# Performance work log

Hardware: AMD Instinct MI355X
Metric: run time of the kernel (lower is better)

Reference implementation:

```python
import jax, jax.numpy as jnp
import numpy as np

B, C, H, W = 2, 128, 64, 64
D_STATE = 16
EXPAND = 2
D_INNER = C * EXPAND          # 256
DT_RANK = -(-C // 16)         # 8
K = 4                         # scan directions
COMPRESS = 3
SQUEEZE = 30
EPS = 1e-5


def layernorm(x, g, b):
    mu = x.mean(-1, keepdims=True)
    xm = x - mu
    var = (xm * xm).mean(-1, keepdims=True)
    return xm * jax.lax.rsqrt(var + EPS) * g + b


def conv2d(x, w, bias, pad):
    y = jax.lax.conv_general_dilated(x, w, (1, 1), ((pad, pad), (pad, pad)),
                                     dimension_numbers=('NCHW', 'OIHW', 'NCHW'))
    return y + bias[None, :, None, None]


def selective_scan(xs, dts, A, Bs, Cs):
    # xs,dts: (B,K,D,L); A: (K,D,N); Bs,Cs: (B,K,N,L)
    dt_t = jnp.moveaxis(dts, -1, 0)
    x_t = jnp.moveaxis(xs, -1, 0)
    B_t = jnp.moveaxis(Bs, -1, 0)
    C_t = jnp.moveaxis(Cs, -1, 0)
    h0 = jnp.zeros(xs.shape[:3] + (A.shape[-1],), xs.dtype)

    def step(h, inp):
        dt_l, x_l, b_l, c_l = inp          # (B,K,D),(B,K,D),(B,K,N),(B,K,N)
        dA = jnp.exp(dt_l[..., None] * A)  # (B,K,D,N)
        h = dA * h + (dt_l * x_l)[..., None] * b_l[:, :, None, :]
        y = jnp.einsum('bkdn,bkn->bkd', h, c_l)
        return h, y

    _, ys = jax.lax.scan(step, h0, (dt_t, x_t, B_t, C_t))
    return jnp.moveaxis(ys, 0, -1)  # (B,K,D,L)


def ss2d(x, p):  # x: (B,H,W,C) -> (B,H,W,C)
    xz = x @ p['in_proj_w'].T
    xc, z = jnp.split(xz, 2, axis=-1)
    xc = xc.transpose(0, 3, 1, 2)  # (B,D,H,W)
    xc = jax.lax.conv_general_dilated(xc, p['conv_w'], (1, 1), ((1, 1), (1, 1)),
                                      feature_group_count=D_INNER,
                                      dimension_numbers=('NCHW', 'OIHW', 'NCHW'))
    xc = jax.nn.silu(xc + p['conv_b'][None, :, None, None])
    b, d, h, w = xc.shape
    L = h * w
    x_hw = xc.reshape(b, d, L)
    x_wh = xc.transpose(0, 1, 3, 2).reshape(b, d, L)
    xs = jnp.stack([x_hw, x_wh, x_hw[..., ::-1], x_wh[..., ::-1]], axis=1)  # (B,4,D,L)
    x_dbl = jnp.einsum('bkdl,kcd->bkcl', xs, p['x_proj_w'])
    dtr, Bs, Cs = jnp.split(x_dbl, [DT_RANK, DT_RANK + D_STATE], axis=2)
    dts = jnp.einsum('bkrl,kdr->bkdl', dtr, p['dt_w'])
    dts = jax.nn.softplus(dts + p['dt_b'][None, :, :, None])
    A = -jnp.exp(p['A_logs']).reshape(K, d, D_STATE)
    ys = selective_scan(xs, dts, A, Bs, Cs)
    ys = ys + xs * p['Ds'].reshape(K, d)[None, :, :, None]
    inv = ys[:, 2:4][..., ::-1]  # undo flipped scans
    wh = lambda t: t.reshape(b, d, w, h).transpose(0, 1, 3, 2).reshape(b, d, L)
    y = ys[:, 0] + inv[:, 0] + wh(ys[:, 1]) + wh(inv[:, 1])
    y = y.transpose(0, 2, 1).reshape(b, h, w, d)
    y = layernorm(y, p['out_norm_g'], p['out_norm_b'])
    y = y * jax.nn.silu(z)
    return y @ p['out_proj_w'].T


def cab(x, p):  # x: (B,C,H,W)
    t = jax.nn.gelu(conv2d(x, p['cab_w1'], p['cab_b1'], 1), approximate=False)
    t = conv2d(t, p['cab_w2'], p['cab_b2'], 1)
    s = t.mean((2, 3), keepdims=True)
    s = jax.nn.relu(conv2d(s, p['ca_w1'], p['ca_b1'], 0))
    s = jax.nn.sigmoid(conv2d(s, p['ca_w2'], p['ca_b2'], 0))
    return t * s


def vss_block(input, p):
    inp = input.transpose(0, 2, 3, 1)  # (B,H,W,C)
    x = inp * p['skip_scale'] + ss2d(layernorm(inp, p['ln1_g'], p['ln1_b']), p)
    c = cab(layernorm(x, p['ln2_g'], p['ln2_b']).transpose(0, 3, 1, 2), p)
    x = x * p['skip_scale2'] + c.transpose(0, 2, 3, 1)
    return x.transpose(0, 3, 1, 2)


def setup_inputs() -> dict:
    key = jax.random.key(0)
    ks = jax.random.split(key, 16)
    rn = lambda i, shp, s=0.02: jax.random.normal(ks[i], shp, jnp.float32) * s
    return {
        'input': jax.random.normal(ks[0], (B, C, H, W), jnp.float32),
        'ln1_g': jnp.ones((C,), jnp.float32), 'ln1_b': jnp.zeros((C,), jnp.float32),
        'skip_scale': jnp.ones((C,), jnp.float32), 'skip_scale2': jnp.ones((C,), jnp.float32),
        'ln2_g': jnp.ones((C,), jnp.float32), 'ln2_b': jnp.zeros((C,), jnp.float32),
        'in_proj_w': rn(1, (2 * D_INNER, C)),
        'conv_w': rn(2, (D_INNER, 1, 3, 3), 0.1),
        'conv_b': jnp.zeros((D_INNER,), jnp.float32),
        'x_proj_w': rn(3, (K, DT_RANK + 2 * D_STATE, D_INNER)),
        'dt_w': rn(4, (K, D_INNER, DT_RANK), 0.1),
        'dt_b': rn(5, (K, D_INNER), 0.1),
        'A_logs': jnp.log(jnp.tile(jnp.arange(1, D_STATE + 1, dtype=jnp.float32), (K * D_INNER, 1))),
        'Ds': jnp.ones((K * D_INNER,), jnp.float32),
        'out_norm_g': jnp.ones((D_INNER,), jnp.float32), 'out_norm_b': jnp.zeros((D_INNER,), jnp.float32),
        'out_proj_w': rn(6, (C, D_INNER)),
        'cab_w1': rn(7, (C // COMPRESS, C, 3, 3), 0.05),
        'cab_b1': jnp.zeros((C // COMPRESS,), jnp.float32),
        'cab_w2': rn(8, (C, C // COMPRESS, 3, 3), 0.05),
        'cab_b2': jnp.zeros((C,), jnp.float32),
        'ca_w1': rn(9, (C // SQUEEZE, C, 1, 1), 0.05),
        'ca_b1': jnp.zeros((C // SQUEEZE,), jnp.float32),
        'ca_w2': rn(10, (C, C // SQUEEZE, 1, 1), 0.05),
        'ca_b2': jnp.zeros((C,), jnp.float32),
    }


def reference(input, ln1_g, ln1_b, skip_scale, skip_scale2, ln2_g, ln2_b,
              in_proj_w, conv_w, conv_b, x_proj_w, dt_w, dt_b, A_logs, Ds,
              out_norm_g, out_norm_b, out_proj_w,
              cab_w1, cab_b1, cab_w2, cab_b2, ca_w1, ca_b1, ca_w2, ca_b2):
    p = dict(ln1_g=ln1_g, ln1_b=ln1_b, skip_scale=skip_scale, skip_scale2=skip_scale2,
             ln2_g=ln2_g, ln2_b=ln2_b, in_proj_w=in_proj_w, conv_w=conv_w, conv_b=conv_b,
             x_proj_w=x_proj_w, dt_w=dt_w, dt_b=dt_b, A_logs=A_logs, Ds=Ds,
             out_norm_g=out_norm_g, out_norm_b=out_norm_b, out_proj_w=out_proj_w,
             cab_w1=cab_w1, cab_b1=cab_b1, cab_w2=cab_w2, cab_b2=cab_b2,
             ca_w1=ca_w1, ca_b1=ca_b1, ca_w2=ca_w2, ca_b2=ca_b2)
    return vss_block(input, p)
```

## Files before the change

### kernel.cpp

```cpp
#include <hip/hip_runtime.h>
#include <math.h>

#define BB 2
#define CC 128
#define HH 64
#define WW 64
#define LL 4096
#define DI 256
#define NS 16
#define KK 4
#define OC1 42

#define NC 256
#define CL 16

#define K3_POS 16
#define BCW 48

__device__ __forceinline__ float sigmoidf_(float x) { return 1.f / (1.f + __expf(-x)); }
__device__ __forceinline__ float siluf_(float x)    { return x * sigmoidf_(x); }

__device__ __forceinline__ int scan_pos(int k, int i) {
  if (k == 0) return i;
  if (k == 1) return ((i & 63) << 6) | (i >> 6);
  if (k == 2) return (LL - 1) - i;
  int j = (LL - 1) - i;
  return ((j & 63) << 6) | (j >> 6);
}

__global__ __launch_bounds__(256) void k1_ln_inproj(
    const float* __restrict__ inp, const float* __restrict__ g, const float* __restrict__ b,
    const float* __restrict__ wproj, float* __restrict__ xcin, float* __restrict__ zbuf) {
  __shared__ float sx[64][132];
  __shared__ float sw[128][68];
  __shared__ float smu[64], srs[64];
  const int tid = threadIdx.x;
  const int rt = blockIdx.x & 3;
  const int pt = blockIdx.x >> 2;
  const int bb = pt >> 6;
  const int pbase = (pt & 63) << 6;

  for (int idx = tid; idx < 64 * CC; idx += 256) {
    int c = idx >> 6, pl = idx & 63;
    sx[pl][c] = inp[((size_t)bb * CC + c) * LL + pbase + pl];
  }
  __syncthreads();
  {
    int pl = tid >> 2, j = tid & 3;
    float s = 0.f, s2 = 0.f;
    for (int c = j; c < CC; c += 4) { float v = sx[pl][c]; s += v; s2 += v * v; }
    s += __shfl_xor(s, 1); s2 += __shfl_xor(s2, 1);
    s += __shfl_xor(s, 2); s2 += __shfl_xor(s2, 2);
    if (j == 0) {
      float mu = s * (1.f / CC);
      smu[pl] = mu;
      srs[pl] = rsqrtf(s2 * (1.f / CC) - mu * mu + 1e-5f);
    }
  }
  __syncthreads();
  for (int idx = tid; idx < 64 * CC; idx += 256) {
    int c = idx & 127, pl = idx >> 7;
    sx[pl][c] = (sx[pl][c] - smu[pl]) * srs[pl] * g[c] + b[c];
  }

  const int pg = tid & 7, rg = tid >> 3;
  float acc[8][4];
#pragma unroll
  for (int j = 0; j < 8; j++)
#pragma unroll
    for (int q = 0; q < 4; q++) acc[j][q] = 0.f;

  for (int kc = 0; kc < CC; kc += 64) {
    __syncthreads();
    for (int idx = tid; idx < 128 * 64; idx += 256) {
      int cl = idx & 63, rl = idx >> 6;
      sw[rl][cl] = wproj[(size_t)(rt * 128 + rl) * CC + kc + cl];
    }
    __syncthreads();
#pragma unroll 4
    for (int i = 0; i < 16; i++) {
      const int k0 = kc + 4 * i, kl0 = 4 * i;
      float4 xv[8], wv[4];
#pragma unroll
      for (int j = 0; j < 8; j++) xv[j] = *(const float4*)&sx[pg + 8 * j][k0];
#pragma unroll
      for (int q = 0; q < 4; q++) wv[q] = *(const float4*)&sw[rg + 32 * q][kl0];
#pragma unroll
      for (int j = 0; j < 8; j++)
#pragma unroll
        for (int q = 0; q < 4; q++) {
          acc[j][q] += xv[j].x * wv[q].x + xv[j].y * wv[q].y
                     + xv[j].z * wv[q].z + xv[j].w * wv[q].w;
        }
    }
  }

  float* buf = (rt < 2) ? xcin : zbuf;
  const int drow = (rt & 1) * 128;
#pragma unroll
  for (int j = 0; j < 8; j++) {
    const int p = pbase + pg + 8 * j;
    float* dst = buf + ((size_t)bb * LL + p) * DI + drow;
#pragma unroll
    for (int q = 0; q < 4; q++) dst[rg + 32 * q] = acc[j][q];
  }
}

__global__ __launch_bounds__(256) void k2_dwconv(
    const float* __restrict__ xcin, const float* __restrict__ cw, const float* __restrict__ cb,
    float* __restrict__ xconv) {
  const int w0 = (blockIdx.x & 7) * 8;
  const int hh = (blockIdx.x >> 3) & 63;
  const int bb = blockIdx.x >> 9;
  const int d = threadIdx.x;

  float wv[9];
#pragma unroll
  for (int kk = 0; kk < 9; kk++) wv[kk] = cw[d * 9 + kk];
  const float bias = cb[d];

  float xin[3][10];
#pragma unroll
  for (int kh = 0; kh < 3; kh++) {
    int r = hh + kh - 1;
    bool vr = (r >= 0 && r < HH);
#pragma unroll
    for (int c = 0; c < 10; c++) {
      int cc2 = w0 + c - 1;
      bool vc = (cc2 >= 0 && cc2 < WW);
      xin[kh][c] = (vr && vc) ? xcin[((size_t)bb * LL + r * WW + cc2) * DI + d] : 0.f;
    }
  }
#pragma unroll
  for (int j = 0; j < 8; j++) {
    float acc = bias;
#pragma unroll
    for (int kh = 0; kh < 3; kh++)
#pragma unroll
      for (int kw = 0; kw < 3; kw++)
        acc += wv[kh * 3 + kw] * xin[kh][j + kw];
    xconv[((size_t)bb * LL + hh * WW + w0 + j) * DI + d] = siluf_(acc);
  }
}

__global__ __launch_bounds__(256) void k3_proj(
    const float* __restrict__ xconv, const float* __restrict__ xpw,
    float* __restrict__ BCbuf) {
  __shared__ float sx[16][68];
  __shared__ float sw[160][68];
  const int tid = threadIdx.x;
  const int bb = blockIdx.x >> 8;
  const int pbase = (blockIdx.x & 255) << 4;

  const int pg = tid & 7, rb = tid >> 3;
  float acc[2][5];
#pragma unroll
  for (int j = 0; j < 2; j++)
#pragma unroll
    for (int q = 0; q < 5; q++) acc[j][q] = 0.f;

  for (int kc = 0; kc < DI; kc += 64) {
    __syncthreads();
    for (int idx = tid; idx < 16 * 64; idx += 256) {
      int cl = idx & 63, pl = idx >> 6;
      sx[pl][cl] = xconv[((size_t)bb * LL + pbase + pl) * DI + kc + cl];
    }
    for (int idx = tid; idx < 160 * 64; idx += 256) {
      int cl = idx & 63, rl = idx >> 6;
      sw[rl][cl] = xpw[(size_t)rl * DI + kc + cl];
    }
    __syncthreads();
#pragma unroll 4
    for (int i = 0; i < 16; i++) {
      float4 xv[2], wv[5];
#pragma unroll
      for (int j = 0; j < 2; j++) xv[j] = *(const float4*)&sx[2 * pg + j][4 * i];
#pragma unroll
      for (int q = 0; q < 5; q++) wv[q] = *(const float4*)&sw[rb + 32 * q][4 * i];
#pragma unroll
      for (int j = 0; j < 2; j++)
#pragma unroll
        for (int q = 0; q < 5; q++) {
          acc[j][q] += xv[j].x * wv[q].x + xv[j].y * wv[q].y
                     + xv[j].z * wv[q].z + xv[j].w * wv[q].w;
        }
    }
  }

#pragma unroll
  for (int j = 0; j < 2; j++) {
    const int p = pbase + 2 * pg + j;
#pragma unroll
    for (int q = 0; q < 5; q++) {
      const int r = rb + 32 * q;
      const int k = r / 40, c0 = r - k * 40;
      BCbuf[((size_t)(bb * KK + k) * LL + p) * BCW + c0] = acc[j][q];
    }
  }
}

__global__ __launch_bounds__(256) void k4a_chunk(
    const float* __restrict__ xconv, const float* __restrict__ BCbuf,
    const float* __restrict__ A_logs, const float* __restrict__ dtw,
    const float* __restrict__ dtb,
    float* __restrict__ csS, float* __restrict__ csB) {
  __shared__ float sBC[CL][26];
  const int d = threadIdx.x;
  const int chunk = blockIdx.x & (NC - 1);
  const int t = blockIdx.x / NC;
  const int k = t & 3;
  const int bb = t >> 2;
  const int bk = bb * KK + k;
  const int base = chunk * CL;

  for (int idx = d; idx < CL * 24; idx += 256) {
    int ii = idx / 24, j = idx - ii * 24;
    int pos = scan_pos(k, base + ii);
    sBC[ii][j] = BCbuf[((size_t)bk * LL + pos) * BCW + j];
  }
  float a[NS];
  bool fast = true;
#pragma unroll
  for (int n = 0; n < NS; n++) {
    a[n] = -__expf(A_logs[((size_t)k * DI + d) * NS + n]);
    fast = fast && (fabsf(a[n] + (float)(n + 1)) < 1e-3f * (n + 1));
  }
  const float* wdt = dtw + ((size_t)k * DI + d) * 8;
  const float4 wd0 = *(const float4*)wdt;
  const float4 wd1 = *(const float4*)(wdt + 4);
  const float bdt = dtb[k * DI + d];
  __syncthreads();

  const float* x_p = xconv + (size_t)bb * LL * DI + d;

  float Bc[NS];
#pragma unroll
  for (int n = 0; n < NS; n++) Bc[n] = 0.f;
  float sumdt = 0.f;

  if (fast) {
#pragma unroll
    for (int half = 0; half < CL / 8; half++) {
      float xvr[8];
#pragma unroll
      for (int j = 0; j < 8; j++)
        xvr[j] = x_p[(size_t)scan_pos(k, base + half * 8 + j) * DI];
#pragma unroll
      for (int j = 0; j < 8; j++) {
        const int ii = half * 8 + j;
        const float* dr = sBC[ii];
        float u = bdt + wd0.x * dr[0] + wd0.y * dr[1] + wd0.z * dr[2] + wd0.w * dr[3]
                      + wd1.x * dr[4] + wd1.y * dr[5] + wd1.z * dr[6] + wd1.w * dr[7];
        float t2 = __expf(u);
        float E = __builtin_amdgcn_rcpf(1.f + t2);
        float dt = u > 20.f ? u : -0.69314718056f * __log2f(E);
        sumdt += dt;
        float dtx = dt * xvr[j];
        float E2 = E * E;
        float dA1 = E, dA2 = E2;
#pragma unroll
        for (int n = 0; n < NS; n += 2) {
          Bc[n] = dA1 * Bc[n] + dtx * sBC[ii][8 + n];
          Bc[n + 1] = dA2 * Bc[n + 1] + dtx * sBC[ii][9 + n];
          dA1 *= E2; dA2 *= E2;
        }
      }
    }
  } else {
#pragma unroll 2
    for (int ii = 0; ii < CL; ii++) {
      int pos = scan_pos(k, base + ii);
      float xv = x_p[(size_t)pos * DI];
      const float* dr = sBC[ii];
      float u = bdt + wd0.x * dr[0] + wd0.y * dr[1] + wd0.z * dr[2] + wd0.w * dr[3]
                    + wd1.x * dr[4] + wd1.y * dr[5] + wd1.z * dr[6] + wd1.w * dr[7];
      float t2 = __expf(u);
      float dt = u > 20.f ? u : log1pf(t2);
      sumdt += dt;
      float dtx = dt * xv;
#pragma unroll
      for (int n = 0; n < NS; n++) {
        float dA = __expf(dt * a[n]);
        Bc[n] = dA * Bc[n] + dtx * sBC[ii][8 + n];
      }
    }
  }
  csS[((size_t)bk * NC + chunk) * DI + d] = sumdt;
  size_t e = ((size_t)(bk * NC + chunk) * NS) * DI + d;
#pragma unroll
  for (int n = 0; n < NS; n++)
    csB[e + (size_t)n * DI] = Bc[n];
}

__global__ __launch_bounds__(256) void k4b_scanchunks(
    const float* __restrict__ csS, const float* __restrict__ csB,
    const float* __restrict__ A_logs, float* __restrict__ hin) {
  const int d = threadIdx.x;
  const int n = blockIdx.x & (NS - 1);
  const int bk = blockIdx.x >> 4;
  const int k = bk & 3;
  const float an = -__expf(A_logs[((size_t)k * DI + d) * NS + n]);
  const size_t strideB = (size_t)NS * DI;
  size_t e = ((size_t)bk * NC * NS + n) * DI + d;
  float H = 0.f;
  for (int c0 = 0; c0 < NC; c0 += 16) {
    float Ea[16], Bv[16];
#pragma unroll
    for (int j = 0; j < 16; j++) {
      Ea[j] = an * csS[((size_t)bk * NC + c0 + j) * DI + d];
      Bv[j] = csB[e + (size_t)j * strideB];
    }
#pragma unroll
    for (int j = 0; j < 16; j++) Ea[j] = __expf(Ea[j]);
#pragma unroll
    for (int j = 0; j < 16; j++) {
      hin[e + (size_t)j * strideB] = H;
      H = Ea[j] * H + Bv[j];
    }
    e += (size_t)16 * strideB;
  }
}

__global__ __launch_bounds__(256) void k4c_scan(
    const float* __restrict__ xconv, const float* __restrict__ BCbuf,
    const float* __restrict__ A_logs, const float* __restrict__ dtw,
    const float* __restrict__ dtb, const float* __restrict__ Ds,
    const float* __restrict__ hin, float* __restrict__ ys) {
  __shared__ float sBC[CL][BCW];
  const int d = threadIdx.x;
  const int chunk = blockIdx.x & (NC - 1);
  const int t = blockIdx.x / NC;
  const int k = t & 3;
  const int bb = t >> 2;
  const int bk = bb * KK + k;
  const int base = chunk * CL;

  for (int idx = d; idx < CL * 40; idx += 256) {
    int ii = idx / 40, j = idx - ii * 40;
    int pos = scan_pos(k, base + ii);
    sBC[ii][j] = BCbuf[((size_t)bk * LL + pos) * BCW + j];
  }
  float a[NS], h[NS];
  bool fast = true;
  const size_t eh = ((size_t)(bk * NC + chunk) * NS) * DI + d;
#pragma unroll
  for (int n = 0; n < NS; n++) {
    a[n] = -__expf(A_logs[((size_t)k * DI + d) * NS + n]);
    fast = fast && (fabsf(a[n] + (float)(n + 1)) < 1e-3f * (n + 1));
    h[n] = hin[eh + (size_t)n * DI];
  }
  const float* wdt = dtw + ((size_t)k * DI + d) * 8;
  const float4 wd0 = *(const float4*)wdt;
  const float4 wd1 = *(const float4*)(wdt + 4);
  const float bdt = dtb[k * DI + d];
  const float Dd = Ds[k * DI + d];
  __syncthreads();

  const float* x_p = xconv + (size_t)bb * LL * DI + d;
  float* ys_p = ys + (size_t)bk * LL * DI + d;

  if (fast) {
#pragma unroll
    for (int half = 0; half < CL / 8; half++) {
      float xvr[8];
#pragma unroll
      for (int j = 0; j < 8; j++)
        xvr[j] = x_p[(size_t)scan_pos(k, base + half * 8 + j) * DI];
#pragma unroll
      for (int j = 0; j < 8; j++) {
        const int ii = half * 8 + j;
        const float* dr = sBC[ii];
        float u = bdt + wd0.x * dr[0] + wd0.y * dr[1] + wd0.z * dr[2] + wd0.w * dr[3]
                      + wd1.x * dr[4] + wd1.y * dr[5] + wd1.z * dr[6] + wd1.w * dr[7];
        float t2 = __expf(u);
        float E = __builtin_amdgcn_rcpf(1.f + t2);
        float dt = u > 20.f ? u : -0.69314718056f * __log2f(E);
        float dtx = dt * xvr[j];
        float y = xvr[j] * Dd;
        float E2 = E * E;
        float dA1 = E, dA2 = E2;
#pragma unroll
        for (int n = 0; n < NS; n += 2) {
          h[n] = dA1 * h[n] + dtx * sBC[ii][8 + n];
          y += h[n] * sBC[ii][24 + n];
          h[n + 1] = dA2 * h[n + 1] + dtx * sBC[ii][9 + n];
          y += h[n + 1] * sBC[ii][25 + n];
          dA1 *= E2; dA2 *= E2;
        }
        ys_p[(size_t)scan_pos(k, base + ii) * DI] = y;
      }
    }
  } else {
#pragma unroll 2
    for (int ii = 0; ii < CL; ii++) {
      int pos = scan_pos(k, base + ii);
      float xv = x_p[(size_t)pos * DI];
      const float* dr = sBC[ii];
      float u = bdt + wd0.x * dr[0] + wd0.y * dr[1] + wd0.z * dr[2] + wd0.w * dr[3]
                    + wd1.x * dr[4] + wd1.y * dr[5] + wd1.z * dr[6] + wd1.w * dr[7];
      float t2 = __expf(u);
      float dt = u > 20.f ? u : log1pf(t2);
      float dtx = dt * xv;
      float y = xv * Dd;
#pragma unroll
      for (int n = 0; n < NS; n++) {
        float dA = __expf(dt * a[n]);
        h[n] = dA * h[n] + dtx * sBC[ii][8 + n];
        y += h[n] * sBC[ii][24 + n];
      }
      ys_p[(size_t)pos * DI] = y;
    }
  }
}

__global__ __launch_bounds__(256) void k5_fused(
    const float* __restrict__ ys, const float* __restrict__ zbuf,
    const float* __restrict__ ong, const float* __restrict__ onb,
    const float* __restrict__ opw,
    const float* __restrict__ inp, const float* __restrict__ sk,
    const float* __restrict__ g2, const float* __restrict__ b2,
    float* __restrict__ xres, float* __restrict__ ln2) {
  __shared__ float sy[16][260];
  __shared__ float sw[128][68];
  __shared__ float sr[16][132];
  __shared__ float smu[16], srs[16];
  const int tid = threadIdx.x;
  const int bb = blockIdx.x >> 8;
  const int pbase = (blockIdx.x & 255) << 4;

  for (int idx = tid; idx < 16 * DI; idx += 256) {
    int d = idx & 255, pl = idx >> 8;
    size_t o0 = (((size_t)bb * KK + 0) * LL + pbase + pl) * DI + d;
    const size_t st = (size_t)LL * DI;
    sy[pl][d] = ys[o0] + ys[o0 + st] + ys[o0 + 2 * st] + ys[o0 + 3 * st];
  }
  __syncthreads();
  {
    int pl = tid >> 4, j = tid & 15;
    float s = 0.f, s2 = 0.f;
    for (int d = j; d < DI; d += 16) { float v = sy[pl][d]; s += v; s2 += v * v; }
#pragma unroll
    for (int m = 1; m < 16; m <<= 1) { s += __shfl_xor(s, m); s2 += __shfl_xor(s2, m); }
    if (j == 0) {
      float mu = s * (1.f / DI);
      smu[pl] = mu;
      srs[pl] = rsqrtf(s2 * (1.f / DI) - mu * mu + 1e-5f);
    }
  }
  __syncthreads();
  for (int idx = tid; idx < 16 * DI; idx += 256) {
    int d = idx & 255, pl = idx >> 8;
    float zv = zbuf[((size_t)bb * LL + pbase + pl) * DI + d];
    sy[pl][d] = ((sy[pl][d] - smu[pl]) * srs[pl] * ong[d] + onb[d]) * siluf_(zv);
  }

  const int pg = tid & 7, rb = tid >> 3;
  float acc[2][4];
#pragma unroll
  for (int j = 0; j < 2; j++)
#pragma unroll
    for (int q = 0; q < 4; q++) acc[j][q] = 0.f;

  for (int kc = 0; kc < DI; kc += 64) {
    __syncthreads();
    for (int idx = tid; idx < 128 * 64; idx += 256) {
      int cl = idx & 63, rl = idx >> 6;
      sw[rl][cl] = opw[(size_t)rl * DI + kc + cl];
    }
    __syncthreads();
#pragma unroll 4
    for (int i = 0; i < 16; i++) {
      float4 xv[2], wv[4];
#pragma unroll
      for (int j = 0; j < 2; j++) xv[j] = *(const float4*)&sy[2 * pg + j][kc + 4 * i];
#pragma unroll
      for (int q = 0; q < 4; q++) wv[q] = *(const float4*)&sw[rb + 32 * q][4 * i];
#pragma unroll
      for (int j = 0; j < 2; j++)
#pragma unroll
        for (int q = 0; q < 4; q++) {
          acc[j][q] += xv[j].x * wv[q].x + xv[j].y * wv[q].y
                     + xv[j].z * wv[q].z + xv[j].w * wv[q].w;
        }
    }
  }

#pragma unroll
  for (int j = 0; j < 2; j++) {
    const int p = pbase + 2 * pg + j;
#pragma unroll
    for (int q = 0; q < 4; q++) {
      const int c = rb + 32 * q;
      float r = inp[((size_t)bb * CC + c) * LL + p] * sk[c] + acc[j][q];
      xres[((size_t)bb * LL + p) * CC + c] = r;
      sr[2 * pg + j][c] = r;
    }
  }
  __syncthreads();
  {
    int pl = tid >> 4, jj = tid & 15;
    float s = 0.f, s2 = 0.f;
    for (int c = jj; c < CC; c += 16) { float v = sr[pl][c]; s += v; s2 += v * v; }
#pragma unroll
    for (int m = 1; m < 16; m <<= 1) { s += __shfl_xor(s, m); s2 += __shfl_xor(s2, m); }
    if (jj == 0) {
      float mu = s * (1.f / CC);
      smu[pl] = mu;
      srs[pl] = rsqrtf(s2 * (1.f / CC) - mu * mu + 1e-5f);
    }
  }
  __syncthreads();
  for (int idx = tid; idx < 16 * CC; idx += 256) {
    int pl = idx & 15, c = idx >> 4;
    ln2[((size_t)bb * CC + c) * LL + pbase + pl] =
        (sr[pl][c] - smu[pl]) * srs[pl] * g2[c] + b2[c];
  }
}

__global__ __launch_bounds__(256) void k6a_conv1(
    const float* __restrict__ ln2, const float* __restrict__ w1,
    float* __restrict__ pc1) {
  __shared__ float sIn[16][6][68];
  __shared__ float sw[16 * 9 * OC1];
  const int tid = threadIdx.x;
  const int icq = blockIdx.x & 7;
  const int h4  = (blockIdx.x >> 3) & 15;
  const int bb  = blockIdx.x >> 7;
  const int icb = icq * 16;

  for (int idx = tid; idx < 16 * 6 * 66; idx += 256) {
    int i = idx / 396, rem = idx % 396;
    int rr = rem / 66, j = rem % 66;
    int r = h4 * 4 + rr - 1, c2 = j - 1;
    float v = 0.f;
    if (r >= 0 && r < HH && c2 >= 0 && c2 < WW)
      v = ln2[((size_t)bb * CC + icb + i) * LL + r * WW + c2];
    sIn[i][rr][j] = v;
  }
  for (int idx = tid; idx < OC1 * 16 * 9; idx += 256) {
    int oc = idx / 144, rem = idx % 144;
    int i = rem / 9, kk = rem % 9;
    sw[(i * 9 + kk) * OC1 + oc] = w1[((size_t)oc * CC + icb + i) * 9 + kk];
  }
  __syncthreads();

  const int wq = tid & 7, hq = (tid >> 3) & 3, ocg = tid >> 5;
  float acc[6][8];
#pragma unroll
  for (int q = 0; q < 6; q++)
#pragma unroll
    for (int ww = 0; ww < 8; ww++) acc[q][ww] = 0.f;

  for (int i = 0; i < 16; i++) {
    float xin[3][10];
#pragma unroll
    for (int kh = 0; kh < 3; kh++)
#pragma unroll
      for (int j = 0; j < 10; j++) xin[kh][j] = sIn[i][hq + kh][wq * 8 + j];
#pragma unroll
    for (int q = 0; q < 6; q++) {
      int oc = ocg + 8 * q;
      if (oc >= OC1) break;
      float wv[9];
#pragma unroll
      for (int kk = 0; kk < 9; kk++) wv[kk] = sw[(i * 9 + kk) * OC1 + oc];
#pragma unroll
      for (int kh = 0; kh < 3; kh++)
#pragma unroll
        for (int kw = 0; kw < 3; kw++)
#pragma unroll
          for (int ww = 0; ww < 8; ww++)
            acc[q][ww] += wv[kh * 3 + kw] * xin[kh][ww + kw];
    }
  }

  const int hrow = h4 * 4 + hq;
#pragma unroll
  for (int q = 0; q < 6; q++) {
    int oc = ocg + 8 * q;
    if (oc >= OC1) break;
    float* dst = pc1 + (((size_t)icq * BB + bb) * OC1 + oc) * LL + hrow * WW + wq * 8;
    *(float4*)dst       = make_float4(acc[q][0], acc[q][1], acc[q][2], acc[q][3]);
    *(float4*)(dst + 4) = make_float4(acc[q][4], acc[q][5], acc[q][6], acc[q][7]);
  }
}

__global__ __launch_bounds__(256) void k6b_reduce(
    const float* __restrict__ pc1, const float* __restrict__ b1,
    float* __restrict__ t1) {
  const int oc = blockIdx.x % OC1;
  const int bb = blockIdx.x / OC1;
  const float bias = b1[oc];
  const size_t st = (size_t)BB * OC1 * LL;
  const float* src = pc1 + ((size_t)bb * OC1 + oc) * LL;
  float* dst = t1 + ((size_t)bb * OC1 + oc) * LL;
  for (int i = threadIdx.x; i < LL / 4; i += 256) {
    float4 s = ((const float4*)src)[i];
#pragma unroll
    for (int icq = 1; icq < 8; icq++) {
      float4 v = *(const float4*)(src + (size_t)icq * st + i * 4);
      s.x += v.x; s.y += v.y; s.z += v.z; s.w += v.w;
    }
    float r[4] = {s.x + bias, s.y + bias, s.z + bias, s.w + bias};
#pragma unroll
    for (int q = 0; q < 4; q++)
      r[q] = 0.5f * r[q] * (1.f + erff(r[q] * 0.70710678118654752f));
    ((float4*)dst)[i] = make_float4(r[0], r[1], r[2], r[3]);
  }
}

__global__ __launch_bounds__(256) void k7_conv2(
    const float* __restrict__ t1, const float* __restrict__ w2,
    float* __restrict__ pc2) {
  __shared__ float sIn[21][4][68];
  __shared__ float swT[32 * 196];
  const int tid = threadIdx.x;
  const int icq = blockIdx.x & 1;
  const int h2  = (blockIdx.x >> 1) & 31;
  const int ocq = (blockIdx.x >> 6) & 3;
  const int bb  = blockIdx.x >> 8;
  const int icb = icq * 21;

  for (int idx = tid; idx < 21 * 4 * 66; idx += 256) {
    int i = idx / 264, rem = idx % 264;
    int rr = rem / 66, j = rem % 66;
    int r = h2 * 2 + rr - 1, c2 = j - 1;
    float v = 0.f;
    if (r >= 0 && r < HH && c2 >= 0 && c2 < WW)
      v = t1[((size_t)bb * OC1 + icb + i) * LL + r * WW + c2];
    sIn[i][rr][j] = v;
  }
  for (int idx = tid; idx < 32 * 189; idx += 256) {
    int ol = idx / 189, ikk = idx % 189;
    swT[ol * 196 + ikk] = w2[(size_t)(ocq * 32 + ol) * (OC1 * 9) + icb * 9 + ikk];
  }
  __syncthreads();

  const int wq = tid & 7, hq = (tid >> 3) & 1, ocg = tid >> 4;
  float acc[2][8];
#pragma unroll
  for (int q = 0; q < 2; q++)
#pragma unroll
    for (int ww = 0; ww < 8; ww++) acc[q][ww] = 0.f;

  for (int i = 0; i < 21; i++) {
    float xin[3][10];
#pragma unroll
    for (int kh = 0; kh < 3; kh++)
#pragma unroll
      for (int j = 0; j < 10; j++) xin[kh][j] = sIn[i][hq + kh][wq * 8 + j];
#pragma unroll
    for (int q = 0; q < 2; q++) {
      int ol = ocg + 16 * q;
      float wv[9];
#pragma unroll
      for (int kk = 0; kk < 9; kk++) wv[kk] = swT[ol * 196 + i * 9 + kk];
#pragma unroll
      for (int kh = 0; kh < 3; kh++)
#pragma unroll
        for (int kw = 0; kw < 3; kw++)
#pragma unroll
          for (int ww = 0; ww < 8; ww++)
            acc[q][ww] += wv[kh * 3 + kw] * xin[kh][ww + kw];
    }
  }

  const int hrow = h2 * 2 + hq;
#pragma unroll
  for (int q = 0; q < 2; q++) {
    int oc = ocq * 32 + ocg + 16 * q;
    float* dst = pc2 + (((size_t)icq * BB + bb) * CC + oc) * LL + hrow * WW + wq * 8;
    *(float4*)dst       = make_float4(acc[q][0], acc[q][1], acc[q][2], acc[q][3]);
    *(float4*)(dst + 4) = make_float4(acc[q][4], acc[q][5], acc[q][6], acc[q][7]);
  }
}

__global__ __launch_bounds__(256) void k8_mean(
    const float* __restrict__ pc2, const float* __restrict__ b2,
    float* __restrict__ t2, float* __restrict__ smean) {
  __shared__ float red[4];
  const int bc = blockIdx.x;
  const int bb = bc >> 7, c = bc & 127;
  const float bias = b2[c];
  const size_t st = (size_t)BB * CC * LL;
  const float* src = pc2 + ((size_t)bb * CC + c) * LL;
  float* dst = t2 + (size_t)bc * LL;
  float s = 0.f;
  for (int i = threadIdx.x; i < LL / 4; i += 256) {
    float4 v0 = ((const float4*)src)[i];
    float4 v1 = *(const float4*)(src + st + i * 4);
    float4 r = make_float4(v0.x + v1.x + bias, v0.y + v1.y + bias,
                           v0.z + v1.z + bias, v0.w + v1.w + bias);
    ((float4*)dst)[i] = r;
    s += r.x + r.y + r.z + r.w;
  }
#pragma unroll
  for (int m = 1; m < 64; m <<= 1) s += __shfl_xor(s, m);
  if ((threadIdx.x & 63) == 0) red[threadIdx.x >> 6] = s;
  __syncthreads();
  if (threadIdx.x == 0) smean[bc] = (red[0] + red[1] + red[2] + red[3]) * (1.f / LL);
}

__global__ __launch_bounds__(256) void k10_final(
    const float* __restrict__ xres, const float* __restrict__ t2,
    const float* __restrict__ smean,
    const float* __restrict__ cw1, const float* __restrict__ cb1,
    const float* __restrict__ cw2, const float* __restrict__ cb2,
    const float* __restrict__ sk2, float* __restrict__ out) {
  __shared__ float mid[4];
  const int tid = threadIdx.x;
  const int bc = blockIdx.x;
  const int bb = bc >> 7, c = bc & 127;

  {
    const int wv = tid >> 6, ln = tid & 63;
    float s = cw1[wv * CC + ln] * smean[bb * CC + ln]
            + cw1[wv * CC + 64 + ln] * smean[bb * CC + 64 + ln];
#pragma unroll
    for (int m = 1; m < 64; m <<= 1) s += __shfl_xor(s, m);
    if (ln == 0) mid[wv] = fmaxf(s + cb1[wv], 0.f);
  }
  __syncthreads();
  float a = cb2[c];
#pragma unroll
  for (int m = 0; m < 4; m++) a += cw2[c * 4 + m] * mid[m];
  const float sv = sigmoidf_(a);

  const float ss = sk2[c];
  const float* t2r = t2 + (size_t)bc * LL;
  float* outr = out + (size_t)bc * LL;
  for (int i = tid; i < LL; i += 256)
    outr[i] = xres[((size_t)bb * LL + i) * CC + c] * ss + t2r[i] * sv;
}


extern "C" void kernel_launch(void* const* d_in, const int* in_sizes, int n_in,
                              void* d_out, int out_size, void* d_ws, size_t ws_size,
                              hipStream_t stream) {
  const float* input      = (const float*)d_in[0];
  const float* ln1_g      = (const float*)d_in[1];
  const float* ln1_b      = (const float*)d_in[2];
  const float* skip_scale = (const float*)d_in[3];
  const float* skip_scale2= (const float*)d_in[4];
  const float* ln2_g      = (const float*)d_in[5];
  const float* ln2_b      = (const float*)d_in[6];
  const float* in_proj_w  = (const float*)d_in[7];
  const float* conv_w     = (const float*)d_in[8];
  const float* conv_b     = (const float*)d_in[9];
  const float* x_proj_w   = (const float*)d_in[10];
  const float* dt_w       = (const float*)d_in[11];
  const float* dt_b       = (const float*)d_in[12];
  const float* A_logs     = (const float*)d_in[13];
  const float* Ds         = (const float*)d_in[14];
  const float* out_norm_g = (const float*)d_in[15];
  const float* out_norm_b = (const float*)d_in[16];
  const float* out_proj_w = (const float*)d_in[17];
  const float* cab_w1     = (const float*)d_in[18];
  const float* cab_b1     = (const float*)d_in[19];
  const float* cab_w2     = (const float*)d_in[20];
  const float* cab_b2     = (const float*)d_in[21];
  const float* ca_w1      = (const float*)d_in[22];
  const float* ca_b1      = (const float*)d_in[23];
  const float* ca_w2      = (const float*)d_in[24];
  const float* ca_b2      = (const float*)d_in[25];

  float* ws = (float*)d_ws;
  float* xcin  = ws;
  float* zbuf  = xcin + (size_t)BB * LL * DI;
  float* xconv = zbuf + (size_t)BB * LL * DI;
  float* BCbuf = xconv + (size_t)BB * LL * DI;
  float* ysb   = BCbuf + (size_t)BB * KK * LL * BCW;
  float* xres  = ysb + (size_t)BB * KK * LL * DI;
  float* ln2b  = xres + (size_t)BB * LL * CC;
  float* t1b   = ln2b + (size_t)BB * CC * LL;
  float* t2b   = t1b + (size_t)BB * OC1 * LL;
  float* smean = t2b + (size_t)BB * CC * LL;
  float* hinbuf= smean + BB * CC;
  float* csS   = hinbuf + (size_t)BB * KK * NC * NS * DI;
  float* csB   = ysb;
  float* pc1   = ysb;
  float* pc2   = ysb + (size_t)3 * 1024 * 1024;

  k1_ln_inproj<<<512, 256, 0, stream>>>(input, ln1_g, ln1_b, in_proj_w, xcin, zbuf);
  k2_dwconv<<<BB * HH * (WW / 8), 256, 0, stream>>>(xcin, conv_w, conv_b, xconv);
  k3_proj<<<BB * (LL / K3_POS), 256, 0, stream>>>(xconv, x_proj_w, BCbuf);
  k4a_chunk<<<BB * KK * NC, 256, 0, stream>>>(xconv, BCbuf, A_logs, dt_w, dt_b, csS, csB);
  k4b_scanchunks<<<BB * KK * NS, 256, 0, stream>>>(csS, csB, A_logs, hinbuf);
  k4c_scan<<<BB * KK * NC, 256, 0, stream>>>(xconv, BCbuf, A_logs, dt_w, dt_b, Ds, hinbuf, ysb);
  k5_fused<<<BB * (LL / 16), 256, 0, stream>>>(ysb, zbuf, out_norm_g, out_norm_b, out_proj_w,
                                               input, skip_scale, ln2_g, ln2_b, xres, ln2b);
  k6a_conv1<<<BB * 16 * 8, 256, 0, stream>>>(ln2b, cab_w1, pc1);
  k6b_reduce<<<BB * OC1, 256, 0, stream>>>(pc1, cab_b1, t1b);
  k7_conv2<<<BB * 4 * 32 * 2, 256, 0, stream>>>(t1b, cab_w2, pc2);
  k8_mean<<<BB * CC, 256, 0, stream>>>(pc2, cab_b2, t2b, smean);
  k10_final<<<BB * CC, 256, 0, stream>>>(xres, t2b, smean, ca_w1, ca_b1, ca_w2, ca_b2,
                                         skip_scale2, (float*)d_out);
}
```

Baseline: 246.4 us.

## Store residual channel-major and drop split-K partials in second CAB conv

The residual is now written channel-major from the LayerNorm loop of the fused output-projection kernel, so the final kernel reads it contiguously instead of with a stride of 128. The second CAB convolution no longer splits input channels into two partial buffers. Each block covers all 42 input channels for 16 output channels, adds the bias and writes t2 directly, so the mean kernel only reduces. This removes one partial-sum round trip and the strided gather, but each conv2 thread now holds fewer output channels, which lowers weight and input reuse per load.

Measured after the change: 256.5 us. 4.1% more time.

```diff
diff --git a/kernel.cpp b/kernel.cpp
--- a/kernel.cpp
+++ b/kernel.cpp
@@ -419,7 +419,7 @@
     const float* __restrict__ opw,
     const float* __restrict__ inp, const float* __restrict__ sk,
     const float* __restrict__ g2, const float* __restrict__ b2,
-    float* __restrict__ xres, float* __restrict__ ln2) {
+    float* __restrict__ xresT, float* __restrict__ ln2) {
   __shared__ float sy[16][260];
   __shared__ float sw[128][68];
   __shared__ float sr[16][132];
@@ -492,7 +492,6 @@
     for (int q = 0; q < 4; q++) {
       const int c = rb + 32 * q;
       float r = inp[((size_t)bb * CC + c) * LL + p] * sk[c] + acc[j][q];
-      xres[((size_t)bb * LL + p) * CC + c] = r;
       sr[2 * pg + j][c] = r;
     }
   }
@@ -512,8 +511,10 @@
   __syncthreads();
   for (int idx = tid; idx < 16 * CC; idx += 256) {
     int pl = idx & 15, c = idx >> 4;
-    ln2[((size_t)bb * CC + c) * LL + pbase + pl] =
-        (sr[pl][c] - smu[pl]) * srs[pl] * g2[c] + b2[c];
+    float r = sr[pl][c];
+    size_t o = ((size_t)bb * CC + c) * LL + pbase + pl;
+    xresT[o] = r;
+    ln2[o] = (r - smu[pl]) * srs[pl] * g2[c] + b2[c];
   }
 }
 
@@ -611,88 +612,71 @@
 
 __global__ __launch_bounds__(256) void k7_conv2(
     const float* __restrict__ t1, const float* __restrict__ w2,
-    float* __restrict__ pc2) {
-  __shared__ float sIn[21][4][68];
-  __shared__ float swT[32 * 196];
+    const float* __restrict__ b2, float* __restrict__ t2) {
+  __shared__ float sIn[OC1][4][68];
+  __shared__ float swT[16 * 388];
   const int tid = threadIdx.x;
-  const int icq = blockIdx.x & 1;
-  const int h2  = (blockIdx.x >> 1) & 31;
-  const int ocq = (blockIdx.x >> 6) & 3;
+  const int h2  = blockIdx.x & 31;
+  const int ocq = (blockIdx.x >> 5) & 7;
   const int bb  = blockIdx.x >> 8;
-  const int icb = icq * 21;
-
-  for (int idx = tid; idx < 21 * 4 * 66; idx += 256) {
+
+  for (int idx = tid; idx < OC1 * 4 * 66; idx += 256) {
     int i = idx / 264, rem = idx % 264;
     int rr = rem / 66, j = rem % 66;
     int r = h2 * 2 + rr - 1, c2 = j - 1;
     float v = 0.f;
     if (r >= 0 && r < HH && c2 >= 0 && c2 < WW)
-      v = t1[((size_t)bb * OC1 + icb + i) * LL + r * WW + c2];
+      v = t1[((size_t)bb * OC1 + i) * LL + r * WW + c2];
     sIn[i][rr][j] = v;
   }
-  for (int idx = tid; idx < 32 * 189; idx += 256) {
-    int ol = idx / 189, ikk = idx % 189;
-    swT[ol * 196 + ikk] = w2[(size_t)(ocq * 32 + ol) * (OC1 * 9) + icb * 9 + ikk];
+  for (int idx = tid; idx < 16 * 378; idx += 256) {
+    int ol = idx / 378, ikk = idx % 378;
+    swT[ol * 388 + ikk] = w2[(size_t)(ocq * 16 + ol) * 378 + ikk];
   }
   __syncthreads();
 
   const int wq = tid & 7, hq = (tid >> 3) & 1, ocg = tid >> 4;
-  float acc[2][8];
-#pragma unroll
-  for (int q = 0; q < 2; q++)
-#pragma unroll
-    for (int ww = 0; ww < 8; ww++) acc[q][ww] = 0.f;
-
-  for (int i = 0; i < 21; i++) {
+  float acc[8];
+#pragma unroll
+  for (int ww = 0; ww < 8; ww++) acc[ww] = 0.f;
+
+  for (int i = 0; i < OC1; i++) {
     float xin[3][10];
 #pragma unroll
     for (int kh = 0; kh < 3; kh++)
 #pragma unroll
       for (int j = 0; j < 10; j++) xin[kh][j] = sIn[i][hq + kh][wq * 8 + j];
-#pragma unroll
-    for (int q = 0; q < 2; q++) {
-      int ol = ocg + 16 * q;
-      float wv[9];
-#pragma unroll
-      for (int kk = 0; kk < 9; kk++) wv[kk] = swT[ol * 196 + i * 9 + kk];
-#pragma unroll
-      for (int kh = 0; kh < 3; kh++)
-#pragma unroll
-        for (int kw = 0; kw < 3; kw++)
-#pragma unroll
-          for (int ww = 0; ww < 8; ww++)
-            acc[q][ww] += wv[kh * 3 + kw] * xin[kh][ww + kw];
-    }
+    float wv[9];
+#pragma unroll
+    for (int kk = 0; kk < 9; kk++) wv[kk] = swT[ocg * 388 + i * 9 + kk];
+#pragma unroll
+    for (int kh = 0; kh < 3; kh++)
+#pragma unroll
+      for (int kw = 0; kw < 3; kw++)
+#pragma unroll
+        for (int ww = 0; ww < 8; ww++)
+          acc[ww] += wv[kh * 3 + kw] * xin[kh][ww + kw];
   }
 
   const int hrow = h2 * 2 + hq;
-#pragma unroll
-  for (int q = 0; q < 2; q++) {
-    int oc = ocq * 32 + ocg + 16 * q;
-    float* dst = pc2 + (((size_t)icq * BB + bb) * CC + oc) * LL + hrow * WW + wq * 8;
-    *(float4*)dst       = make_float4(acc[q][0], acc[q][1], acc[q][2], acc[q][3]);
-    *(float4*)(dst + 4) = make_float4(acc[q][4], acc[q][5], acc[q][6], acc[q][7]);
-  }
+  const int oc = ocq * 16 + ocg;
+  const float bias = b2[oc];
+  float* dst = t2 + ((size_t)bb * CC + oc) * LL + hrow * WW + wq * 8;
+  *(float4*)dst       = make_float4(acc[0] + bias, acc[1] + bias,
+                                    acc[2] + bias, acc[3] + bias);
+  *(float4*)(dst + 4) = make_float4(acc[4] + bias, acc[5] + bias,
+                                    acc[6] + bias, acc[7] + bias);
 }
 
 __global__ __launch_bounds__(256) void k8_mean(
-    const float* __restrict__ pc2, const float* __restrict__ b2,
-    float* __restrict__ t2, float* __restrict__ smean) {
+    const float* __restrict__ t2, float* __restrict__ smean) {
   __shared__ float red[4];
   const int bc = blockIdx.x;
-  const int bb = bc >> 7, c = bc & 127;
-  const float bias = b2[c];
-  const size_t st = (size_t)BB * CC * LL;
-  const float* src = pc2 + ((size_t)bb * CC + c) * LL;
-  float* dst = t2 + (size_t)bc * LL;
+  const float* src = t2 + (size_t)bc * LL;
   float s = 0.f;
   for (int i = threadIdx.x; i < LL / 4; i += 256) {
-    float4 v0 = ((const float4*)src)[i];
-    float4 v1 = *(const float4*)(src + st + i * 4);
-    float4 r = make_float4(v0.x + v1.x + bias, v0.y + v1.y + bias,
-                           v0.z + v1.z + bias, v0.w + v1.w + bias);
-    ((float4*)dst)[i] = r;
-    s += r.x + r.y + r.z + r.w;
+    float4 v = ((const float4*)src)[i];
+    s += v.x + v.y + v.z + v.w;
   }
 #pragma unroll
   for (int m = 1; m < 64; m <<= 1) s += __shfl_xor(s, m);
@@ -702,7 +686,7 @@
 }
 
 __global__ __launch_bounds__(256) void k10_final(
-    const float* __restrict__ xres, const float* __restrict__ t2,
+    const float* __restrict__ xresT, const float* __restrict__ t2,
     const float* __restrict__ smean,
     const float* __restrict__ cw1, const float* __restrict__ cb1,
     const float* __restrict__ cw2, const float* __restrict__ cb2,
@@ -728,9 +712,10 @@
 
   const float ss = sk2[c];
   const float* t2r = t2 + (size_t)bc * LL;
+  const float* xrt = xresT + (size_t)bc * LL;
   float* outr = out + (size_t)bc * LL;
   for (int i = tid; i < LL; i += 256)
-    outr[i] = xres[((size_t)bb * LL + i) * CC + c] * ss + t2r[i] * sv;
+    outr[i] = xrt[i] * ss + t2r[i] * sv;
 }
 
 
@@ -770,8 +755,8 @@
   float* xconv = zbuf + (size_t)BB * LL * DI;
   float* BCbuf = xconv + (size_t)BB * LL * DI;
   float* ysb   = BCbuf + (size_t)BB * KK * LL * BCW;
-  float* xres  = ysb + (size_t)BB * KK * LL * DI;
-  float* ln2b  = xres + (size_t)BB * LL * CC;
+  float* xresT = ysb + (size_t)BB * KK * LL * DI;
+  float* ln2b  = xresT + (size_t)BB * LL * CC;
   float* t1b   = ln2b + (size_t)BB * CC * LL;
   float* t2b   = t1b + (size_t)BB * OC1 * LL;
   float* smean = t2b + (size_t)BB * CC * LL;
@@ -779,7 +764,6 @@
   float* csS   = hinbuf + (size_t)BB * KK * NC * NS * DI;
   float* csB   = ysb;
   float* pc1   = ysb;
-  float* pc2   = ysb + (size_t)3 * 1024 * 1024;
 
   k1_ln_inproj<<<512, 256, 0, stream>>>(input, ln1_g, ln1_b, in_proj_w, xcin, zbuf);
   k2_dwconv<<<BB * HH * (WW / 8), 256, 0, stream>>>(xcin, conv_w, conv_b, xconv);
@@ -788,11 +772,11 @@
   k4b_scanchunks<<<BB * KK * NS, 256, 0, stream>>>(csS, csB, A_logs, hinbuf);
   k4c_scan<<<BB * KK * NC, 256, 0, stream>>>(xconv, BCbuf, A_logs, dt_w, dt_b, Ds, hinbuf, ysb);
   k5_fused<<<BB * (LL / 16), 256, 0, stream>>>(ysb, zbuf, out_norm_g, out_norm_b, out_proj_w,
-                                               input, skip_scale, ln2_g, ln2_b, xres, ln2b);
+                                               input, skip_scale, ln2_g, ln2_b, xresT, ln2b);
   k6a_conv1<<<BB * 16 * 8, 256, 0, stream>>>(ln2b, cab_w1, pc1);
   k6b_reduce<<<BB * OC1, 256, 0, stream>>>(pc1, cab_b1, t1b);
-  k7_conv2<<<BB * 4 * 32 * 2, 256, 0, stream>>>(t1b, cab_w2, pc2);
-  k8_mean<<<BB * CC, 256, 0, stream>>>(pc2, cab_b2, t2b, smean);
-  k10_final<<<BB * CC, 256, 0, stream>>>(xres, t2b, smean, ca_w1, ca_b1, ca_w2, ca_b2,
+  k7_conv2<<<BB * 8 * 32, 256, 0, stream>>>(t1b, cab_w2, cab_b2, t2b);
+  k8_mean<<<BB * CC, 256, 0, stream>>>(t2b, smean);
+  k10_final<<<BB * CC, 256, 0, stream>>>(xresT, t2b, smean, ca_w1, ca_b1, ca_w2, ca_b2,
                                          skip_scale2, (float*)d_out);
 }
```
